# Kernel tuning notes

Measured on AMD Instinct MI355X. Metric: run time of the kernel, lower is better.

Reference implementation:

```python
import jax, jax.numpy as jnp
import numpy as np

PATCH, STRIDE, TOPK, EPS = 16, 8, 8, 1e-8

def _leaky(x):
    return jax.nn.leaky_relu(x, 0.01)

def setup_inputs() -> dict:
    key = jax.random.key(0)
    ks = jax.random.split(key, 12)
    s = 0.05  # small weight scale to avoid tanh saturation
    return {
        "X":      jax.random.normal(ks[0], (16, 4096, 512), jnp.float32),
        "W_enc1": jax.random.normal(ks[1], (512, 256), jnp.float32) * s,
        "b_enc1": jax.random.normal(ks[2], (256,), jnp.float32) * s,
        "W_enc2": jax.random.normal(ks[3], (256, 64), jnp.float32) * s,
        "b_enc2": jax.random.normal(ks[4], (64,), jnp.float32) * s,
        "Wq":     jax.random.normal(ks[5], (64, 64), jnp.float32) * s,
        "Wk":     jax.random.normal(ks[6], (64, 64), jnp.float32) * s,
        "Wv":     jax.random.normal(ks[7], (64, 64), jnp.float32) * s,
        "W_agg":  jax.random.normal(ks[8], (64, 64), jnp.float32) * s,
        "b_agg":  jax.random.normal(ks[9], (64,), jnp.float32) * s,
        "W_dec":  jax.random.normal(ks[10], (64, 512), jnp.float32) * s,
        "b_dec":  jax.random.normal(ks[11], (512,), jnp.float32) * s,
    }

def reference(X, W_enc1, b_enc1, W_enc2, b_enc2, Wq, Wk, Wv, W_agg, b_agg, W_dec, b_dec):
    B, L, D = X.shape
    # var_encoder (dropout-free MLP)
    Xe = _leaky(X @ W_enc1 + b_enc1) @ W_enc2 + b_enc2          # (B, L, d)
    d = Xe.shape[-1]
    # unfold into overlapping patches
    h = (L - PATCH) // STRIDE + 1
    pos = jnp.arange(h)[:, None] * STRIDE + jnp.arange(PATCH)[None, :]  # (h, PATCH)
    patches = Xe[:, pos, :]                                      # (B, h, PATCH, d)
    per_patch = patches.mean(axis=2).reshape(B * h, d)           # (N, d)
    q = per_patch @ Wq
    k = per_patch @ Wk
    v = per_patch @ Wv                                           # (N, hqk)
    qn = q / (jnp.linalg.norm(q, axis=-1, keepdims=True) + EPS)
    kn = k / (jnp.linalg.norm(k, axis=-1, keepdims=True) + EPS)
    # antisymmetric outer product, (N, hqk, hqk)
    M = qn[:, :, None] * kn[:, None, :] - kn[:, :, None] * qn[:, None, :]
    A = jax.nn.relu(jnp.tanh(M))
    n = A.shape[-1]
    # topk pruning along last dim via scatter-style mask
    _, idx = jax.lax.top_k(A, TOPK)                              # (N, n, TOPK)
    mask = jnp.any(idx[..., None] == jnp.arange(n), axis=-2)     # (N, n, n) bool
    A = A * mask.astype(A.dtype)
    A = A / jnp.maximum(A.sum(axis=-1, keepdims=True), EPS)
    Av = jnp.einsum('nij,nj->ni', A, v)                          # (N, hqk)
    # after_agg (dropout = identity in eval)
    z = _leaky(Av @ W_agg + b_agg)                               # (N, d)
    zB = z.reshape(B, h, d)
    # overlap-add fold: each patch writes its (constant-over-time) z to its window
    seg = jnp.broadcast_to(zB[:, :, None, :], (B, h, PATCH, d)).reshape(B, h * PATCH, d)
    flat_pos = pos.reshape(-1)                                   # (h*PATCH,)
    out = jnp.zeros((B, L, d), X.dtype).at[:, flat_pos, :].add(seg)
    counts = jnp.zeros((L,), X.dtype).at[flat_pos].add(1.0)
    out = out / jnp.maximum(counts, 1.0)[None, :, None]
    return out @ W_dec + b_dec                                   # (B, L, D)
```

## Files before the change

kernel.cpp:

```cpp
#include <hip/hip_runtime.h>


typedef __attribute__((ext_vector_type(8))) short short8;
typedef __attribute__((ext_vector_type(4))) float floatx4;

__device__ __forceinline__ unsigned short f2bf(float f) {
    unsigned u = __float_as_uint(f);
    u += 0x7FFFu + ((u >> 16) & 1u);
    return (unsigned short)(u >> 16);
}

__global__ __launch_bounds__(256) void prep_weights(
    const float* __restrict__ W1, const float* __restrict__ W2,
    const float* __restrict__ Wd,
    unsigned short* __restrict__ W1t, unsigned short* __restrict__ W2t,
    unsigned short* __restrict__ Wdt)
{
    int idx = blockIdx.x * 256 + threadIdx.x;
    { int n = idx >> 9, k = idx & 511;  W1t[idx] = f2bf(W1[k * 256 + n]); }
    if (idx < 16384) { int n = idx >> 8, k = idx & 255; W2t[idx] = f2bf(W2[k * 64 + n]); }
    if (idx < 32768) { int n = idx >> 6, k = idx & 63;  Wdt[idx] = f2bf(Wd[k * 512 + n]); }
}

template<int BM, int BN, int WM, int WN, bool AF32, int EPI>
__global__ __launch_bounds__(256) void gemm_kernel(
    const void* __restrict__ Aq, const unsigned short* __restrict__ Bt,
    const float* __restrict__ bias, void* __restrict__ Cq,
    int M, int N, int K, int lda)
{
    constexpr int LDK = 72;
    __shared__ short As[BM * LDK];
    __shared__ short Bs[BN * LDK];

    const int tid  = threadIdx.x;
    const int lane = tid & 63;
    const int w    = tid >> 6;
    constexpr int MWAVES = BM / WM;
    const int wrow = (w % MWAVES) * WM;
    const int wcol = (w / MWAVES) * WN;
    constexpr int MI = WM / 16, NI = WN / 16;
    const int m0 = blockIdx.y * BM;
    const int n0 = blockIdx.x * BN;

    floatx4 acc[MI][NI];
#pragma unroll
    for (int a = 0; a < MI; a++)
#pragma unroll
        for (int bq = 0; bq < NI; bq++) acc[a][bq] = (floatx4){0.f, 0.f, 0.f, 0.f};

    constexpr int EPTA = BM * 64 / 256;
    constexpr int TPRA = 64 / EPTA;
    const int arow  = tid / TPRA;
    const int akseg = (tid % TPRA) * EPTA;
    constexpr int EPTB = BN * 64 / 256;
    constexpr int TPRB = 64 / EPTB;
    const int brow  = tid / TPRB;
    const int bkseg = (tid % TPRB) * EPTB;

    for (int kt = 0; kt < K; kt += 64) {
        if constexpr (AF32) {
            const float* src = (const float*)Aq + (size_t)(m0 + arow) * lda + kt + akseg;
            short* dst = &As[arow * LDK + akseg];
#pragma unroll
            for (int u = 0; u < EPTA; u += 8) {
                float4 f0 = *(const float4*)(src + u);
                float4 f1 = *(const float4*)(src + u + 4);
                short8 o;
                o[0] = (short)f2bf(f0.x); o[1] = (short)f2bf(f0.y);
                o[2] = (short)f2bf(f0.z); o[3] = (short)f2bf(f0.w);
                o[4] = (short)f2bf(f1.x); o[5] = (short)f2bf(f1.y);
                o[6] = (short)f2bf(f1.z); o[7] = (short)f2bf(f1.w);
                *(short8*)(dst + u) = o;
            }
        } else {
            const unsigned short* src = (const unsigned short*)Aq + (size_t)(m0 + arow) * lda + kt + akseg;
            short* dst = &As[arow * LDK + akseg];
#pragma unroll
            for (int u = 0; u < EPTA; u += 8)
                *(short8*)(dst + u) = *(const short8*)(src + u);
        }
        {
            const unsigned short* src = Bt + (size_t)(n0 + brow) * K + kt + bkseg;
            short* dst = &Bs[brow * LDK + bkseg];
#pragma unroll
            for (int u = 0; u < EPTB; u += 8)
                *(short8*)(dst + u) = *(const short8*)(src + u);
        }
        __syncthreads();

#pragma unroll
        for (int ks = 0; ks < 2; ks++) {
            const int koff = ks * 32 + (lane >> 4) * 8;
            short8 af[MI], bf[NI];
#pragma unroll
            for (int mi = 0; mi < MI; mi++)
                af[mi] = *(const short8*)&As[(wrow + mi * 16 + (lane & 15)) * LDK + koff];
#pragma unroll
            for (int ni = 0; ni < NI; ni++)
                bf[ni] = *(const short8*)&Bs[(wcol + ni * 16 + (lane & 15)) * LDK + koff];
#pragma unroll
            for (int mi = 0; mi < MI; mi++)
#pragma unroll
                for (int ni = 0; ni < NI; ni++)
                    acc[mi][ni] = __builtin_amdgcn_mfma_f32_16x16x32_bf16(
                        af[mi], bf[ni], acc[mi][ni], 0, 0, 0);
        }
        __syncthreads();
    }

#pragma unroll
    for (int mi = 0; mi < MI; mi++) {
#pragma unroll
        for (int ni = 0; ni < NI; ni++) {
            const int col = n0 + wcol + ni * 16 + (lane & 15);
            const float bv = bias[col];
#pragma unroll
            for (int r = 0; r < 4; r++) {
                const int row = m0 + wrow + mi * 16 + (lane >> 4) * 4 + r;
                float v = acc[mi][ni][r] + bv;
                if constexpr (EPI == 0) {
                    v = v > 0.f ? v : 0.01f * v;
                    ((unsigned short*)Cq)[(size_t)row * N + col] = f2bf(v);
                } else {
                    ((float*)Cq)[(size_t)row * N + col] = v;
                }
            }
        }
    }
}

#define TOP8_INS(mv) do { float _x = (mv); float _t;            \
    _t = fmaxf(s0,_x); _x = fminf(s0,_x); s0 = _t;              \
    _t = fmaxf(s1,_x); _x = fminf(s1,_x); s1 = _t;              \
    _t = fmaxf(s2,_x); _x = fminf(s2,_x); s2 = _t;              \
    _t = fmaxf(s3,_x); _x = fminf(s3,_x); s3 = _t;              \
    _t = fmaxf(s4,_x); _x = fminf(s4,_x); s4 = _t;              \
    _t = fmaxf(s5,_x); _x = fminf(s5,_x); s5 = _t;              \
    _t = fmaxf(s6,_x); _x = fminf(s6,_x); s6 = _t;              \
    s7 = fmaxf(s7,_x); } while (0)

__global__ __launch_bounds__(256) void patch_attn(
    const float* __restrict__ Xe,  const float* __restrict__ Wq,
    const float* __restrict__ Wk,  const float* __restrict__ Wv,
    const float* __restrict__ Wagg, const float* __restrict__ bagg,
    float* __restrict__ zout)
{
    __shared__ float sh[4][336];
    const int w    = threadIdx.x >> 6;
    const int lane = threadIdx.x & 63;
    const int n = blockIdx.x * 4 + w;
    const int b = n / 511;
    const int i = n - b * 511;
    float* pp  = &sh[w][0];
    float* qs  = pp + 64;
    float* ksm = pp + 128;
    float* vsm = pp + 192;
    float* avs = pp + 256;

    const float* xb = Xe + ((size_t)(b * 4096 + i * 8)) * 64 + lane;
    float s = 0.f;
#pragma unroll
    for (int p = 0; p < 16; p++) s += xb[(size_t)p * 64];
    pp[lane] = s * 0.0625f;
    __syncthreads();

    float q = 0.f, k = 0.f, v = 0.f;
#pragma unroll 4
    for (int e = 0; e < 64; e += 4) {
        float4 p4 = *(const float4*)&pp[e];
        q = fmaf(p4.x, Wq[(e+0)*64+lane], q); q = fmaf(p4.y, Wq[(e+1)*64+lane], q);
        q = fmaf(p4.z, Wq[(e+2)*64+lane], q); q = fmaf(p4.w, Wq[(e+3)*64+lane], q);
        k = fmaf(p4.x, Wk[(e+0)*64+lane], k); k = fmaf(p4.y, Wk[(e+1)*64+lane], k);
        k = fmaf(p4.z, Wk[(e+2)*64+lane], k); k = fmaf(p4.w, Wk[(e+3)*64+lane], k);
        v = fmaf(p4.x, Wv[(e+0)*64+lane], v); v = fmaf(p4.y, Wv[(e+1)*64+lane], v);
        v = fmaf(p4.z, Wv[(e+2)*64+lane], v); v = fmaf(p4.w, Wv[(e+3)*64+lane], v);
    }
    float sq = q * q, sk = k * k;
#pragma unroll
    for (int o = 1; o < 64; o <<= 1) { sq += __shfl_xor(sq, o); sk += __shfl_xor(sk, o); }
    const float qni = q / (sqrtf(sq) + 1e-8f);
    const float kni = k / (sqrtf(sk) + 1e-8f);
    qs[lane] = qni; ksm[lane] = kni; vsm[lane] = v;
    __syncthreads();

    auto MV = [&](float kj, float qj) { return fmaf(qni, kj, -(kni * qj)); };

    float s0=-1e30f,s1=-1e30f,s2=-1e30f,s3=-1e30f,s4=-1e30f,s5=-1e30f,s6=-1e30f,s7=-1e30f;
#pragma unroll
    for (int j = 0; j < 64; j += 4) {
        float4 k4 = *(const float4*)&ksm[j];
        float4 q4 = *(const float4*)&qs[j];
        TOP8_INS(MV(k4.x, q4.x)); TOP8_INS(MV(k4.y, q4.y));
        TOP8_INS(MV(k4.z, q4.z)); TOP8_INS(MV(k4.w, q4.w));
    }
    const float teff = fmaxf(s7, 1e-37f) * (1.f - 1.2e-7f);

    float ssum = 0.f, av = 0.f;
#pragma unroll
    for (int j = 0; j < 64; j += 4) {
        float4 k4 = *(const float4*)&ksm[j];
        float4 q4 = *(const float4*)&qs[j];
        float4 v4 = *(const float4*)&vsm[j];
#define P2(KJ, QJ, VJ) do { float _m = MV(KJ, QJ); float _x2 = _m * _m;           \
        float _a = _m * (15.f + _x2) * __builtin_amdgcn_rcpf(fmaf(6.f, _x2, 15.f)); \
        float _am = (_m >= teff) ? _a : 0.f;                                       \
        ssum += _am; av = fmaf(_am, (VJ), av); } while (0)
        P2(k4.x, q4.x, v4.x); P2(k4.y, q4.y, v4.y);
        P2(k4.z, q4.z, v4.z); P2(k4.w, q4.w, v4.w);
#undef P2
    }
    avs[lane] = av / fmaxf(ssum, 1e-8f);
    __syncthreads();

    float zc = bagg[lane];
#pragma unroll 4
    for (int e = 0; e < 64; e += 4) {
        float4 a4 = *(const float4*)&avs[e];
        zc = fmaf(a4.x, Wagg[(e+0)*64+lane], zc); zc = fmaf(a4.y, Wagg[(e+1)*64+lane], zc);
        zc = fmaf(a4.z, Wagg[(e+2)*64+lane], zc); zc = fmaf(a4.w, Wagg[(e+3)*64+lane], zc);
    }
    zc = zc > 0.f ? zc : 0.01f * zc;
    zout[(size_t)n * 64 + lane] = zc;
}

__global__ __launch_bounds__(256) void scatter_avg(
    const float* __restrict__ z, unsigned short* __restrict__ zavg)
{
    const int idx = blockIdx.x * 256 + threadIdx.x;
    const int c = idx & 63;
    const int l = (idx >> 6) & 4095;
    const int b = idx >> 18;
    const int g = l >> 3;
    float s = 0.f, cnt = 0.f;
    if (g >= 1)   { s += z[((size_t)(b * 511 + g - 1)) * 64 + c]; cnt += 1.f; }
    if (g <= 510) { s += z[((size_t)(b * 511 + g)) * 64 + c];     cnt += 1.f; }
    zavg[idx] = f2bf(s / cnt);
}

extern "C" void kernel_launch(void* const* d_in, const int* in_sizes, int n_in,
                              void* d_out, int out_size, void* d_ws, size_t ws_size,
                              hipStream_t stream)
{
    const float* X    = (const float*)d_in[0];
    const float* W1   = (const float*)d_in[1];
    const float* b1   = (const float*)d_in[2];
    const float* W2   = (const float*)d_in[3];
    const float* b2   = (const float*)d_in[4];
    const float* Wq   = (const float*)d_in[5];
    const float* Wk   = (const float*)d_in[6];
    const float* Wv   = (const float*)d_in[7];
    const float* Wagg = (const float*)d_in[8];
    const float* bagg = (const float*)d_in[9];
    const float* Wd   = (const float*)d_in[10];
    const float* bd   = (const float*)d_in[11];

    char* ws = (char*)d_ws;
    unsigned short* hidden = (unsigned short*)(ws);
    float*          Xe     = (float*)(ws + 33554432);
    float*          z      = (float*)(ws + 50331648);
    unsigned short* zavg   = (unsigned short*)(ws + 52424704);
    unsigned short* W1t    = (unsigned short*)(ws + 60813312);
    unsigned short* W2t    = (unsigned short*)(ws + 61075456);
    unsigned short* Wdt    = (unsigned short*)(ws + 61108224);
    float* out = (float*)d_out;

    prep_weights<<<512, 256, 0, stream>>>(W1, W2, Wd, W1t, W2t, Wdt);

    gemm_kernel<128,128,64,64,true,0><<<dim3(2,512), 256, 0, stream>>>(
        X, W1t, b1, hidden, 65536, 256, 512, 512);
    gemm_kernel<128,64,32,64,false,1><<<dim3(1,512), 256, 0, stream>>>(
        hidden, W2t, b2, Xe, 65536, 64, 256, 256);
    patch_attn<<<2044, 256, 0, stream>>>(Xe, Wq, Wk, Wv, Wagg, bagg, z);
    scatter_avg<<<16384, 256, 0, stream>>>(z, zavg);
    gemm_kernel<128,128,64,64,false,1><<<dim3(4,512), 256, 0, stream>>>(
        zavg, Wdt, bd, out, 65536, 512, 64, 64);
}
```

Baseline: 344.7 us.

## Prefetch GEMM tiles into registers, stage epilogue via LDS, switch to fp16

The GEMM kernel now loads the next K tile into registers while MFMAs run on the current shared tile, giving a simple software pipeline. The epilogue writes accumulators into shared memory in 32-row chunks and then issues coalesced float4/half4 global stores, replacing scattered scalar stores. Operands also move from bf16 with manual rounding to fp16 with hardware conversion and fp16 MFMA, which makes conversion cheaper. The costs are more registers, extra barriers in the epilogue, and fp16 range or precision risk on the activations.

```diff
diff --git a/kernel.cpp b/kernel.cpp
--- a/kernel.cpp
+++ b/kernel.cpp
@@ -1,36 +1,34 @@
 #include <hip/hip_runtime.h>
 
 
-typedef __attribute__((ext_vector_type(8))) short short8;
+typedef __attribute__((ext_vector_type(8))) _Float16 half8;
+typedef __attribute__((ext_vector_type(4))) _Float16 half4;
 typedef __attribute__((ext_vector_type(4))) float floatx4;
 
-__device__ __forceinline__ unsigned short f2bf(float f) {
-    unsigned u = __float_as_uint(f);
-    u += 0x7FFFu + ((u >> 16) & 1u);
-    return (unsigned short)(u >> 16);
-}
+__device__ __forceinline__ _Float16 f2h(float f) { return (_Float16)f; }
 
 __global__ __launch_bounds__(256) void prep_weights(
     const float* __restrict__ W1, const float* __restrict__ W2,
     const float* __restrict__ Wd,
-    unsigned short* __restrict__ W1t, unsigned short* __restrict__ W2t,
-    unsigned short* __restrict__ Wdt)
+    _Float16* __restrict__ W1t, _Float16* __restrict__ W2t,
+    _Float16* __restrict__ Wdt)
 {
     int idx = blockIdx.x * 256 + threadIdx.x;
-    { int n = idx >> 9, k = idx & 511;  W1t[idx] = f2bf(W1[k * 256 + n]); }
-    if (idx < 16384) { int n = idx >> 8, k = idx & 255; W2t[idx] = f2bf(W2[k * 64 + n]); }
-    if (idx < 32768) { int n = idx >> 6, k = idx & 63;  Wdt[idx] = f2bf(Wd[k * 512 + n]); }
+    { int n = idx >> 9, k = idx & 511;  W1t[idx] = f2h(W1[k * 256 + n]); }
+    if (idx < 16384) { int n = idx >> 8, k = idx & 255; W2t[idx] = f2h(W2[k * 64 + n]); }
+    if (idx < 32768) { int n = idx >> 6, k = idx & 63;  Wdt[idx] = f2h(Wd[k * 512 + n]); }
 }
 
 template<int BM, int BN, int WM, int WN, bool AF32, int EPI>
 __global__ __launch_bounds__(256) void gemm_kernel(
-    const void* __restrict__ Aq, const unsigned short* __restrict__ Bt,
+    const void* __restrict__ Aq, const _Float16* __restrict__ Bt,
     const float* __restrict__ bias, void* __restrict__ Cq,
     int M, int N, int K, int lda)
 {
     constexpr int LDK = 72;
-    __shared__ short As[BM * LDK];
-    __shared__ short Bs[BN * LDK];
+    __shared__ _Float16 As[BM * LDK];
+    __shared__ _Float16 Bs[BN * LDK];
+    static_assert(32 * BN * 4 <= BM * LDK * 2, "epilogue chunk must fit in As");
 
     const int tid  = threadIdx.x;
     const int lane = tid & 63;
@@ -57,73 +55,118 @@
     const int brow  = tid / TPRB;
     const int bkseg = (tid % TPRB) * EPTB;
 
-    for (int kt = 0; kt < K; kt += 64) {
+    const float*    Af = (const float*)Aq;
+    const _Float16* Ah = (const _Float16*)Aq;
+
+    float4 pa[AF32 ? EPTA / 4 : 1];
+    half8  paq[AF32 ? 1 : EPTA / 8];
+    half8  pb[EPTB / 8];
+
+    auto loadA = [&](int kt) {
         if constexpr (AF32) {
-            const float* src = (const float*)Aq + (size_t)(m0 + arow) * lda + kt + akseg;
-            short* dst = &As[arow * LDK + akseg];
-#pragma unroll
-            for (int u = 0; u < EPTA; u += 8) {
-                float4 f0 = *(const float4*)(src + u);
-                float4 f1 = *(const float4*)(src + u + 4);
-                short8 o;
-                o[0] = (short)f2bf(f0.x); o[1] = (short)f2bf(f0.y);
-                o[2] = (short)f2bf(f0.z); o[3] = (short)f2bf(f0.w);
-                o[4] = (short)f2bf(f1.x); o[5] = (short)f2bf(f1.y);
-                o[6] = (short)f2bf(f1.z); o[7] = (short)f2bf(f1.w);
-                *(short8*)(dst + u) = o;
+            const float* s = Af + (size_t)(m0 + arow) * lda + kt + akseg;
+#pragma unroll
+            for (int u = 0; u < EPTA / 4; u++) pa[u] = *(const float4*)(s + 4 * u);
+        } else {
+            const _Float16* s = Ah + (size_t)(m0 + arow) * lda + kt + akseg;
+#pragma unroll
+            for (int u = 0; u < EPTA / 8; u++) paq[u] = *(const half8*)(s + 8 * u);
+        }
+    };
+    auto loadB = [&](int kt) {
+        const _Float16* s = Bt + (size_t)(n0 + brow) * K + kt + bkseg;
+#pragma unroll
+        for (int u = 0; u < EPTB / 8; u++) pb[u] = *(const half8*)(s + 8 * u);
+    };
+    auto stage = [&]() {
+        _Float16* d = &As[arow * LDK + akseg];
+        if constexpr (AF32) {
+#pragma unroll
+            for (int u = 0; u < EPTA / 8; u++) {
+                float4 f0 = pa[2 * u], f1 = pa[2 * u + 1];
+                half8 o;
+                o[0] = f2h(f0.x); o[1] = f2h(f0.y); o[2] = f2h(f0.z); o[3] = f2h(f0.w);
+                o[4] = f2h(f1.x); o[5] = f2h(f1.y); o[6] = f2h(f1.z); o[7] = f2h(f1.w);
+                *(half8*)(d + 8 * u) = o;
             }
         } else {
-            const unsigned short* src = (const unsigned short*)Aq + (size_t)(m0 + arow) * lda + kt + akseg;
-            short* dst = &As[arow * LDK + akseg];
-#pragma unroll
-            for (int u = 0; u < EPTA; u += 8)
-                *(short8*)(dst + u) = *(const short8*)(src + u);
-        }
-        {
-            const unsigned short* src = Bt + (size_t)(n0 + brow) * K + kt + bkseg;
-            short* dst = &Bs[brow * LDK + bkseg];
-#pragma unroll
-            for (int u = 0; u < EPTB; u += 8)
-                *(short8*)(dst + u) = *(const short8*)(src + u);
-        }
+#pragma unroll
+            for (int u = 0; u < EPTA / 8; u++) *(half8*)(d + 8 * u) = paq[u];
+        }
+        _Float16* db = &Bs[brow * LDK + bkseg];
+#pragma unroll
+        for (int u = 0; u < EPTB / 8; u++) *(half8*)(db + 8 * u) = pb[u];
+    };
+
+    loadA(0); loadB(0);
+    for (int kt = 0; kt < K; kt += 64) {
+        stage();
         __syncthreads();
-
+        if (kt + 64 < K) { loadA(kt + 64); loadB(kt + 64); }
 #pragma unroll
         for (int ks = 0; ks < 2; ks++) {
             const int koff = ks * 32 + (lane >> 4) * 8;
-            short8 af[MI], bf[NI];
+            half8 af[MI], bf[NI];
 #pragma unroll
             for (int mi = 0; mi < MI; mi++)
-                af[mi] = *(const short8*)&As[(wrow + mi * 16 + (lane & 15)) * LDK + koff];
+                af[mi] = *(const half8*)&As[(wrow + mi * 16 + (lane & 15)) * LDK + koff];
 #pragma unroll
             for (int ni = 0; ni < NI; ni++)
-                bf[ni] = *(const short8*)&Bs[(wcol + ni * 16 + (lane & 15)) * LDK + koff];
+                bf[ni] = *(const half8*)&Bs[(wcol + ni * 16 + (lane & 15)) * LDK + koff];
 #pragma unroll
             for (int mi = 0; mi < MI; mi++)
 #pragma unroll
                 for (int ni = 0; ni < NI; ni++)
-                    acc[mi][ni] = __builtin_amdgcn_mfma_f32_16x16x32_bf16(
+                    acc[mi][ni] = __builtin_amdgcn_mfma_f32_16x16x32_f16(
                         af[mi], bf[ni], acc[mi][ni], 0, 0, 0);
         }
         __syncthreads();
     }
 
-#pragma unroll
-    for (int mi = 0; mi < MI; mi++) {
-#pragma unroll
-        for (int ni = 0; ni < NI; ni++) {
-            const int col = n0 + wcol + ni * 16 + (lane & 15);
-            const float bv = bias[col];
-#pragma unroll
-            for (int r = 0; r < 4; r++) {
-                const int row = m0 + wrow + mi * 16 + (lane >> 4) * 4 + r;
-                float v = acc[mi][ni][r] + bv;
-                if constexpr (EPI == 0) {
-                    v = v > 0.f ? v : 0.01f * v;
-                    ((unsigned short*)Cq)[(size_t)row * N + col] = f2bf(v);
-                } else {
-                    ((float*)Cq)[(size_t)row * N + col] = v;
+    float bvv[NI];
+#pragma unroll
+    for (int ni = 0; ni < NI; ni++) bvv[ni] = bias[n0 + wcol + ni * 16 + (lane & 15)];
+
+    float* Cs = (float*)As;
+#pragma unroll
+    for (int c = 0; c < BM / 32; c++) {
+        __syncthreads();
+        constexpr int DUMMY = 0; (void)DUMMY;
+        {
+            const int own_wrow = ((c * 32) / WM) * WM;
+            if (wrow == own_wrow) {
+                constexpr int CPW = 32 < WM ? 32 : WM;
+#pragma unroll
+                for (int mm = 0; mm < CPW / 16; mm++) {
+                    const int mi = ((c * 32) % WM) / 16 + mm;
+#pragma unroll
+                    for (int ni = 0; ni < NI; ni++) {
+#pragma unroll
+                        for (int r = 0; r < 4; r++) {
+                            const int lr  = mm * 16 + (lane >> 4) * 4 + r;
+                            const int col = wcol + ni * 16 + (lane & 15);
+                            Cs[lr * BN + col] = acc[mi][ni][r] + bvv[ni];
+                        }
+                    }
                 }
+            }
+        }
+        __syncthreads();
+#pragma unroll
+        for (int u = 0; u < (32 * BN) / 1024; u++) {
+            const int idx = (u * 256 + tid) * 4;
+            const int lr = idx / BN, col = idx - lr * BN;
+            float4 vv = *(const float4*)&Cs[idx];
+            const size_t go = (size_t)(m0 + c * 32 + lr) * N + n0 + col;
+            if constexpr (EPI == 0) {
+                half4 hv;
+                hv[0] = f2h(vv.x > 0.f ? vv.x : 0.01f * vv.x);
+                hv[1] = f2h(vv.y > 0.f ? vv.y : 0.01f * vv.y);
+                hv[2] = f2h(vv.z > 0.f ? vv.z : 0.01f * vv.z);
+                hv[3] = f2h(vv.w > 0.f ? vv.w : 0.01f * vv.w);
+                *(half4*)((_Float16*)Cq + go) = hv;
+            } else {
+                *(float4*)((float*)Cq + go) = vv;
             }
         }
     }
@@ -224,7 +267,7 @@
 }
 
 __global__ __launch_bounds__(256) void scatter_avg(
-    const float* __restrict__ z, unsigned short* __restrict__ zavg)
+    const float* __restrict__ z, _Float16* __restrict__ zavg)
 {
     const int idx = blockIdx.x * 256 + threadIdx.x;
     const int c = idx & 63;
@@ -234,7 +277,7 @@
     float s = 0.f, cnt = 0.f;
     if (g >= 1)   { s += z[((size_t)(b * 511 + g - 1)) * 64 + c]; cnt += 1.f; }
     if (g <= 510) { s += z[((size_t)(b * 511 + g)) * 64 + c];     cnt += 1.f; }
-    zavg[idx] = f2bf(s / cnt);
+    zavg[idx] = f2h(s / cnt);
 }
 
 extern "C" void kernel_launch(void* const* d_in, const int* in_sizes, int n_in,
@@ -255,13 +298,13 @@
     const float* bd   = (const float*)d_in[11];
 
     char* ws = (char*)d_ws;
-    unsigned short* hidden = (unsigned short*)(ws);
-    float*          Xe     = (float*)(ws + 33554432);
-    float*          z      = (float*)(ws + 50331648);
-    unsigned short* zavg   = (unsigned short*)(ws + 52424704);
-    unsigned short* W1t    = (unsigned short*)(ws + 60813312);
-    unsigned short* W2t    = (unsigned short*)(ws + 61075456);
-    unsigned short* Wdt    = (unsigned short*)(ws + 61108224);
+    _Float16* hidden = (_Float16*)(ws);
+    float*    Xe     = (float*)(ws + 33554432);
+    float*    z      = (float*)(ws + 50331648);
+    _Float16* zavg   = (_Float16*)(ws + 52424704);
+    _Float16* W1t    = (_Float16*)(ws + 60813312);
+    _Float16* W2t    = (_Float16*)(ws + 61075456);
+    _Float16* Wdt    = (_Float16*)(ws + 61108224);
     float* out = (float*)d_out;
 
     prep_weights<<<512, 256, 0, stream>>>(W1, W2, Wd, W1t, W2t, Wdt);
```

Result: no change. 341.2 us (-1.0%).
